# Optimization experiments

Hardware: AMD Instinct MI355X
Metric: run time of the kernel (lower is better)

Reference implementation:

```python
import jax, jax.numpy as jnp
import numpy as np

DIM_H = 128
HEADS = 8
HEAD_DIM = DIM_H // HEADS
N_NODES = 40000
N_EDGES = 640000
BN_EPS = 1e-5


def setup_inputs() -> dict:
    key = jax.random.key(0)
    ks = jax.random.split(key, 16)
    s = 0.05
    x = jax.random.normal(ks[0], (N_NODES, DIM_H), dtype=jnp.float32)
    edge_index = jax.random.randint(ks[1], (2, N_EDGES), 0, N_NODES, dtype=jnp.int64)
    p = lambda k, shp: jax.random.normal(k, shp, dtype=jnp.float32) * s
    return {
        "x": x,
        "edge_index": edge_index,
        "Wk": p(ks[2], (DIM_H, DIM_H)), "bk": p(ks[3], (DIM_H,)),
        "Wv": p(ks[4], (DIM_H, DIM_H)), "bv": p(ks[5], (DIM_H,)),
        "Wo": p(ks[6], (DIM_H, DIM_H)), "bo": p(ks[7], (DIM_H,)),
        "bn1_g": jnp.ones((DIM_H,), jnp.float32), "bn1_b": jnp.zeros((DIM_H,), jnp.float32),
        "W1": p(ks[8], (2 * DIM_H, DIM_H)), "b1": p(ks[9], (2 * DIM_H,)),
        "W2": p(ks[10], (DIM_H, 2 * DIM_H)), "b2": p(ks[11], (DIM_H,)),
        "bn2_g": jnp.ones((DIM_H,), jnp.float32), "bn2_b": jnp.zeros((DIM_H,), jnp.float32),
    }


def _batchnorm(h, gamma, beta):
    # BatchNorm1d in training mode: per-feature batch mean / biased var over nodes
    mu = jnp.mean(h, axis=0)
    var = jnp.mean((h - mu) ** 2, axis=0)
    return (h - mu) * jax.lax.rsqrt(var + BN_EPS) * gamma + beta


def _sparse_attn(x, edge_index, Wk, bk, Wv, bv, Wo, bo):
    N = x.shape[0]
    src, dst = edge_index[0], edge_index[1]
    K = (x @ Wk.T + bk).reshape(N, HEADS, HEAD_DIM)
    V = (x @ Wv.T + bv).reshape(N, HEADS, HEAD_DIM)
    Q = x.reshape(N, HEADS, HEAD_DIM)  # query is raw h (no projection)
    # per-edge scores [E, H]
    scores = jnp.sum(K[src] * Q[dst], axis=-1) / np.sqrt(HEAD_DIM).astype(np.float32)
    # segment softmax over destination nodes (pyg_softmax)
    m = jax.ops.segment_max(scores, dst, num_segments=N)
    e = jnp.exp(scores - m[dst])
    denom = jax.ops.segment_sum(e, dst, num_segments=N)
    attn = e / (denom[dst] + 1e-16)  # [E, H]
    messages = V[src] * attn[:, :, None]  # [E, H, D]
    out = jax.ops.segment_sum(messages, dst, num_segments=N)  # [N, H, D]
    return out.reshape(N, DIM_H) @ Wo.T + bo


def reference(x, edge_index, Wk, bk, Wv, bv, Wo, bo, bn1_g, bn1_b,
              W1, b1, W2, b2, bn2_g, bn2_b):
    h_attn = _sparse_attn(x, edge_index, Wk, bk, Wv, bv, Wo, bo)
    h = _batchnorm(x + h_attn, bn1_g, bn1_b)
    ff = jax.nn.relu(h @ W1.T + b1) @ W2.T + b2
    h = _batchnorm(h + ff, bn2_g, bn2_b)
    return h
```

## Files before the change

kernel.cpp:

```cpp
#include <hip/hip_runtime.h>

#define DIM 128
#define NSHARD 8

typedef __attribute__((ext_vector_type(2))) float f32x2;
typedef __attribute__((ext_vector_type(4))) _Float16 half4;
typedef __attribute__((ext_vector_type(8))) _Float16 half8;
typedef __attribute__((ext_vector_type(4))) float f32x4;

#define HP 136
#define UP 264

__device__ __forceinline__ unsigned char to_fp8(float v) {
  return (unsigned char)(__builtin_amdgcn_cvt_pk_fp8_f32(v, v, 0, false) & 0xff);
}

__global__ __launch_bounds__(256) void conv_wall(const float* __restrict__ Wk,
    const float* __restrict__ Wv, const float* __restrict__ Wo,
    const float* __restrict__ W1, const float* __restrict__ W2,
    _Float16* __restrict__ Wkh, _Float16* __restrict__ Wvh,
    _Float16* __restrict__ Woh, _Float16* __restrict__ W1h,
    _Float16* __restrict__ W2h, int* __restrict__ cnt, float* __restrict__ stats,
    int N) {
  int i = blockIdx.x * 256 + threadIdx.x;
  int nth = gridDim.x * 256;
  if (i < 16384) Wkh[i] = (_Float16)Wk[i];
  else if (i < 32768) Wvh[i - 16384] = (_Float16)Wv[i - 16384];
  else if (i < 49152) Woh[i - 32768] = (_Float16)Wo[i - 32768];
  else if (i < 81920) W1h[i - 49152] = (_Float16)W1[i - 49152];
  else if (i < 114688) W2h[i - 81920] = (_Float16)W2[i - 81920];
  for (int j = i; j < N * NSHARD; j += nth) cnt[j] = 0;
  if (i < 512) stats[i] = 0.f;
}

__global__ __launch_bounds__(256) void kv_mfma(const float* __restrict__ x,
    const _Float16* __restrict__ Wkh, const float* __restrict__ bk,
    const _Float16* __restrict__ Wvh, const float* __restrict__ bv,
    unsigned char* __restrict__ KV8, int N) {
  __shared__ _Float16 xs[64 * HP];
  int tid = threadIdx.x;
  int base = blockIdx.x * 64;
  int lane = tid & 63, w = tid >> 6;
  int l15 = lane & 15, quad = lane >> 4;

  for (int i = tid; i < 64 * 32; i += 256) {
    int m = i >> 5, c4 = i & 31;
    float4 tv = ((const float4*)x)[(size_t)(base + m) * 32 + c4];
    half4 hv;
    hv.x = (_Float16)tv.x; hv.y = (_Float16)tv.y;
    hv.z = (_Float16)tv.z; hv.w = (_Float16)tv.w;
    *(half4*)&xs[m * HP + c4 * 4] = hv;
  }
  __syncthreads();

  half8 afr[4][4];
#pragma unroll
  for (int mt = 0; mt < 4; mt++)
#pragma unroll
    for (int ks = 0; ks < 4; ks++)
      afr[mt][ks] = *(const half8*)&xs[(mt * 16 + l15) * HP + ks * 32 + quad * 8];

  const _Float16* W = (w < 2) ? Wkh : Wvh;
  const float* bias = (w < 2) ? bk : bv;
  int voff = (w < 2) ? 0 : 4;
  int c0 = (w & 1) * 64;

#pragma unroll
  for (int nt = 0; nt < 4; nt++) {
    int f = c0 + nt * 16 + l15;
    half8 bfr[4];
#pragma unroll
    for (int ks = 0; ks < 4; ks++)
      bfr[ks] = *(const half8*)&W[(size_t)f * 128 + ks * 32 + quad * 8];
    f32x4 acc[4];
#pragma unroll
    for (int mt = 0; mt < 4; mt++) acc[mt] = (f32x4){0.f, 0.f, 0.f, 0.f};
#pragma unroll
    for (int ks = 0; ks < 4; ks++)
#pragma unroll
      for (int mt = 0; mt < 4; mt++)
        acc[mt] = __builtin_amdgcn_mfma_f32_16x16x32_f16(afr[mt][ks], bfr[ks],
                                                          acc[mt], 0, 0, 0);
    float bb = bias[f];
    int fo = (f >> 2) * 8 + (f & 3) + voff;
#pragma unroll
    for (int mt = 0; mt < 4; mt++)
#pragma unroll
      for (int r = 0; r < 4; r++)
        KV8[(size_t)(base + mt * 16 + quad * 4 + r) * 256 + fo] =
            to_fp8(acc[mt][r] + bb);
  }
}

__global__ __launch_bounds__(256) void hist_rank(const int* __restrict__ ei,
    int* __restrict__ cnt, int* __restrict__ rank, int N, int E) {
  int e = blockIdx.x * 256 + threadIdx.x;
  if (e < E) rank[e] = atomicAdd(&cnt[(e & (NSHARD - 1)) * N + ei[E + e]], 1);
}

__global__ __launch_bounds__(256) void scanA(const int* __restrict__ cnt,
    int* __restrict__ rs, int* __restrict__ bsum, int N) {
  __shared__ int s[256];
  int t = threadIdx.x;
  int i = blockIdx.x * 256 + t;
  int v = 0;
  if (i < N)
#pragma unroll
    for (int sh = 0; sh < NSHARD; sh++) v += cnt[sh * N + i];
  s[t] = v;
  __syncthreads();
  for (int off = 1; off < 256; off <<= 1) {
    int add = (t >= off) ? s[t - off] : 0;
    __syncthreads();
    s[t] += add;
    __syncthreads();
  }
  if (i < N) rs[i] = s[t] - v;
  if (t == 255) bsum[blockIdx.x] = s[t];
}

__global__ __launch_bounds__(256) void scanB(int* __restrict__ bsum, int nb) {
  __shared__ int s[256];
  int t = threadIdx.x;
  int v = (t < nb) ? bsum[t] : 0;
  s[t] = v;
  __syncthreads();
  for (int off = 1; off < 256; off <<= 1) {
    int add = (t >= off) ? s[t - off] : 0;
    __syncthreads();
    s[t] += add;
    __syncthreads();
  }
  if (t < nb) bsum[t] = s[t] - v;
}

__global__ __launch_bounds__(256) void scanC(int* __restrict__ rs,
    const int* __restrict__ bsum, const int* __restrict__ cnt,
    int* __restrict__ rs_shard, int N, int E) {
  int i = blockIdx.x * 256 + threadIdx.x;
  if (i < N) {
    int b = rs[i] + bsum[blockIdx.x];
    rs[i] = b;
#pragma unroll
    for (int sh = 0; sh < NSHARD; sh++) {
      rs_shard[sh * N + i] = b;
      b += cnt[sh * N + i];
    }
  }
  if (i == 0) rs[N] = E;
}

__global__ __launch_bounds__(256) void scatter2(const int* __restrict__ ei,
    const int* __restrict__ rs_shard, const int* __restrict__ rank,
    int* __restrict__ esrc, int N, int E) {
  int e = blockIdx.x * 256 + threadIdx.x;
  if (e < E)
    esrc[rs_shard[(e & (NSHARD - 1)) * N + ei[E + e]] + rank[e]] = ei[e];
}

__global__ __launch_bounds__(256) void attn_agg(const unsigned char* __restrict__ KV8,
    const float* __restrict__ x, const int* __restrict__ rs,
    const int* __restrict__ esrc, _Float16* __restrict__ attn16, int N) {
  int wave = threadIdx.x >> 6, lane = threadIdx.x & 63;
  int n = blockIdx.x * 4 + wave;
  if (n >= N) return;
  int l = lane & 31, s = lane >> 5;
  float4 q = *(const float4*)&x[(size_t)n * DIM + 4 * l];
  int beg = rs[n], end = rs[n + 1];
  float a0 = 0.f, a1 = 0.f, a2 = 0.f, a3 = 0.f, dloc = 0.f;
  for (int e = beg + s; e < end; e += 8) {
    bool hh[4];
    int ss[4];
#pragma unroll
    for (int u = 0; u < 4; u++) hh[u] = (e + 2 * u) < end;
    ss[0] = esrc[e];
#pragma unroll
    for (int u = 1; u < 4; u++) ss[u] = hh[u] ? esrc[e + 2 * u] : ss[0];
    uint2 kv[4];
#pragma unroll
    for (int u = 0; u < 4; u++)
      kv[u] = *(const uint2*)&KV8[(size_t)ss[u] * 256 + 8 * l];
    float p[4];
#pragma unroll
    for (int u = 0; u < 4; u++) {
      f32x2 k01 = __builtin_amdgcn_cvt_pk_f32_fp8(kv[u].x, false);
      f32x2 k23 = __builtin_amdgcn_cvt_pk_f32_fp8(kv[u].x, true);
      p[u] = k01[0] * q.x + k01[1] * q.y + k23[0] * q.z + k23[1] * q.w;
    }
#pragma unroll
    for (int u = 0; u < 4; u++) p[u] += __shfl_xor(p[u], 1);
#pragma unroll
    for (int u = 0; u < 4; u++) p[u] += __shfl_xor(p[u], 2);
#pragma unroll
    for (int u = 0; u < 4; u++) {
      float ev = hh[u] ? __expf(p[u] * 0.25f) : 0.f;
      dloc += ev;
      f32x2 v01 = __builtin_amdgcn_cvt_pk_f32_fp8(kv[u].y, false);
      f32x2 v23 = __builtin_amdgcn_cvt_pk_f32_fp8(kv[u].y, true);
      a0 += ev * v01[0];
      a1 += ev * v01[1];
      a2 += ev * v23[0];
      a3 += ev * v23[1];
    }
  }
  dloc += __shfl_xor(dloc, 32);
  a0 += __shfl_xor(a0, 32);
  a1 += __shfl_xor(a1, 32);
  a2 += __shfl_xor(a2, 32);
  a3 += __shfl_xor(a3, 32);
  if (s == 0) {
    float inv = 1.0f / (dloc + 1e-16f);
    half4 o;
    o.x = (_Float16)(a0 * inv);
    o.y = (_Float16)(a1 * inv);
    o.z = (_Float16)(a2 * inv);
    o.w = (_Float16)(a3 * inv);
    *(half4*)&attn16[(size_t)n * DIM + 4 * l] = o;
  }
}

__global__ __launch_bounds__(256) void o_proj_mfma(const _Float16* __restrict__ attn16,
    const float* __restrict__ x, const _Float16* __restrict__ Woh,
    const float* __restrict__ bo, float* __restrict__ t,
    float* __restrict__ stats, int N) {
  __shared__ _Float16 as16[64 * HP];
  int tid = threadIdx.x;
  int base = blockIdx.x * 64;
  int lane = tid & 63, w = tid >> 6;
  int l15 = lane & 15, quad = lane >> 4;

  for (int i = tid; i < 64 * 16; i += 256) {
    int m = i >> 4, c8 = i & 15;
    *(half8*)&as16[m * HP + c8 * 8] =
        ((const half8*)attn16)[(size_t)(base + m) * 16 + c8];
  }
  __syncthreads();

  half8 afr[4][4];
#pragma unroll
  for (int mt = 0; mt < 4; mt++)
#pragma unroll
    for (int ks = 0; ks < 4; ks++)
      afr[mt][ks] = *(const half8*)&as16[(mt * 16 + l15) * HP + ks * 32 + quad * 8];

  int c0 = w * 32;
  f32x4 acc[4][2];
#pragma unroll
  for (int mt = 0; mt < 4; mt++)
#pragma unroll
    for (int nt = 0; nt < 2; nt++) acc[mt][nt] = (f32x4){0.f, 0.f, 0.f, 0.f};
#pragma unroll
  for (int ks = 0; ks < 4; ks++) {
    half8 b[2];
#pragma unroll
    for (int nt = 0; nt < 2; nt++)
      b[nt] = *(const half8*)&Woh[(size_t)(c0 + nt * 16 + l15) * 128 + ks * 32 +
                                  quad * 8];
#pragma unroll
    for (int mt = 0; mt < 4; mt++)
#pragma unroll
      for (int nt = 0; nt < 2; nt++)
        acc[mt][nt] =
            __builtin_amdgcn_mfma_f32_16x16x32_f16(afr[mt][ks], b[nt], acc[mt][nt], 0, 0, 0);
  }

#pragma unroll
  for (int nt = 0; nt < 2; nt++) {
    int f = c0 + nt * 16 + l15;
    float bb = bo[f];
    float s = 0.f, q = 0.f;
#pragma unroll
    for (int mt = 0; mt < 4; mt++) {
#pragma unroll
      for (int r = 0; r < 4; r++) {
        int row = mt * 16 + quad * 4 + r;
        float tv = acc[mt][nt][r] + bb + x[(size_t)(base + row) * DIM + f];
        t[(size_t)(base + row) * DIM + f] = tv;
        s += tv;
        q += tv * tv;
      }
    }
    s += __shfl_xor(s, 16);
    s += __shfl_xor(s, 32);
    q += __shfl_xor(q, 16);
    q += __shfl_xor(q, 32);
    if (quad == 0) {
      atomicAdd(&stats[f], s);
      atomicAdd(&stats[128 + f], q);
    }
  }
}

__global__ __launch_bounds__(256) void ffn_mfma(const float* __restrict__ t,
    const float* __restrict__ stats1, const float* __restrict__ g1,
    const float* __restrict__ bb1, const _Float16* __restrict__ W1h,
    const float* __restrict__ b1, const _Float16* __restrict__ W2h,
    const float* __restrict__ b2, float* __restrict__ z,
    float* __restrict__ stats2, float invN, int N) {
  __shared__ _Float16 hs[64 * HP];
  __shared__ _Float16 us[64 * UP];
  __shared__ float cf[256];
  int tid = threadIdx.x;
  int base = blockIdx.x * 64;
  int lane = tid & 63, w = tid >> 6;
  int l15 = lane & 15, quad = lane >> 4;

  if (tid < 128) {
    float mu = stats1[tid] * invN;
    float var = stats1[128 + tid] * invN - mu * mu;
    float a = rsqrtf(var + 1e-5f) * g1[tid];
    cf[tid] = a;
    cf[128 + tid] = bb1[tid] - mu * a;
  }
  __syncthreads();

  for (int i = tid; i < 64 * 32; i += 256) {
    int m = i >> 5, c4 = i & 31;
    float4 tv = ((const float4*)t)[(size_t)(base + m) * 32 + c4];
    float4 ca = ((const float4*)cf)[c4];
    float4 cc = ((const float4*)cf)[32 + c4];
    half4 hv;
    hv.x = (_Float16)(tv.x * ca.x + cc.x);
    hv.y = (_Float16)(tv.y * ca.y + cc.y);
    hv.z = (_Float16)(tv.z * ca.z + cc.z);
    hv.w = (_Float16)(tv.w * ca.w + cc.w);
    *(half4*)&hs[m * HP + c4 * 4] = hv;
  }
  __syncthreads();

  int n0 = w * 64;
  half8 afr[4][4];
#pragma unroll
  for (int mt = 0; mt < 4; mt++)
#pragma unroll
    for (int ks = 0; ks < 4; ks++)
      afr[mt][ks] = *(const half8*)&hs[(mt * 16 + l15) * HP + ks * 32 + quad * 8];

#pragma unroll
  for (int nt = 0; nt < 4; nt++) {
    int n = n0 + nt * 16 + l15;
    half8 bfr[4];
#pragma unroll
    for (int ks = 0; ks < 4; ks++)
      bfr[ks] = *(const half8*)&W1h[(size_t)n * 128 + ks * 32 + quad * 8];
    f32x4 acc[4];
#pragma unroll
    for (int mt = 0; mt < 4; mt++) acc[mt] = (f32x4){0.f, 0.f, 0.f, 0.f};
#pragma unroll
    for (int ks = 0; ks < 4; ks++)
#pragma unroll
      for (int mt = 0; mt < 4; mt++)
        acc[mt] = __builtin_amdgcn_mfma_f32_16x16x32_f16(afr[mt][ks], bfr[ks],
                                                          acc[mt], 0, 0, 0);
    float bias = b1[n];
#pragma unroll
    for (int mt = 0; mt < 4; mt++)
#pragma unroll
      for (int r = 0; r < 4; r++)
        us[(mt * 16 + quad * 4 + r) * UP + n] =
            (_Float16)fmaxf(acc[mt][r] + bias, 0.f);
  }
  __syncthreads();

  int n2 = w * 32;
  f32x4 acc2[4][2];
#pragma unroll
  for (int mt = 0; mt < 4; mt++)
#pragma unroll
    for (int nt = 0; nt < 2; nt++) acc2[mt][nt] = (f32x4){0.f, 0.f, 0.f, 0.f};
  for (int ks = 0; ks < 8; ks++) {
    half8 a[4], b[2];
#pragma unroll
    for (int mt = 0; mt < 4; mt++)
      a[mt] = *(const half8*)&us[(mt * 16 + l15) * UP + ks * 32 + quad * 8];
#pragma unroll
    for (int nt = 0; nt < 2; nt++)
      b[nt] = *(const half8*)&W2h[(size_t)(n2 + nt * 16 + l15) * 256 + ks * 32 +
                                  quad * 8];
#pragma unroll
    for (int mt = 0; mt < 4; mt++)
#pragma unroll
      for (int nt = 0; nt < 2; nt++)
        acc2[mt][nt] =
            __builtin_amdgcn_mfma_f32_16x16x32_f16(a[mt], b[nt], acc2[mt][nt], 0, 0, 0);
  }

#pragma unroll
  for (int nt = 0; nt < 2; nt++) {
    int f = n2 + nt * 16 + l15;
    float bz = b2[f];
    float s = 0.f, q = 0.f;
#pragma unroll
    for (int mt = 0; mt < 4; mt++) {
#pragma unroll
      for (int r = 0; r < 4; r++) {
        int row = mt * 16 + quad * 4 + r;
        float hv = (float)hs[row * HP + f];
        float zv = hv + acc2[mt][nt][r] + bz;
        z[(size_t)(base + row) * DIM + f] = zv;
        s += zv;
        q += zv * zv;
      }
    }
    s += __shfl_xor(s, 16);
    s += __shfl_xor(s, 32);
    q += __shfl_xor(q, 16);
    q += __shfl_xor(q, 32);
    if (quad == 0) {
      atomicAdd(&stats2[f], s);
      atomicAdd(&stats2[128 + f], q);
    }
  }
}

__global__ __launch_bounds__(256) void final_apply(const float* __restrict__ z,
    const float* __restrict__ stats2, const float* __restrict__ g2,
    const float* __restrict__ bb2, float* __restrict__ out, float invN,
    int total4) {
  __shared__ float cf[256];
  int tid = threadIdx.x;
  if (tid < 128) {
    float mu = stats2[tid] * invN;
    float var = stats2[128 + tid] * invN - mu * mu;
    float a = rsqrtf(var + 1e-5f) * g2[tid];
    cf[tid] = a;
    cf[128 + tid] = bb2[tid] - mu * a;
  }
  __syncthreads();
  int i = blockIdx.x * 256 + tid;
  if (i >= total4) return;
  int f = (i * 4) & 127;
  float4 zv = ((const float4*)z)[i];
  float4 o;
  o.x = zv.x * cf[f] + cf[128 + f];
  o.y = zv.y * cf[f + 1] + cf[128 + f + 1];
  o.z = zv.z * cf[f + 2] + cf[128 + f + 2];
  o.w = zv.w * cf[f + 3] + cf[128 + f + 3];
  ((float4*)out)[i] = o;
}

extern "C" void kernel_launch(void* const* d_in, const int* in_sizes, int n_in,
                              void* d_out, int out_size, void* d_ws, size_t ws_size,
                              hipStream_t stream) {
  const float* x = (const float*)d_in[0];
  const int* ei = (const int*)d_in[1];
  const float* Wk = (const float*)d_in[2];
  const float* bk = (const float*)d_in[3];
  const float* Wv = (const float*)d_in[4];
  const float* bv = (const float*)d_in[5];
  const float* Wo = (const float*)d_in[6];
  const float* bo = (const float*)d_in[7];
  const float* bn1_g = (const float*)d_in[8];
  const float* bn1_b = (const float*)d_in[9];
  const float* W1 = (const float*)d_in[10];
  const float* b1 = (const float*)d_in[11];
  const float* W2 = (const float*)d_in[12];
  const float* b2 = (const float*)d_in[13];
  const float* bn2_g = (const float*)d_in[14];
  const float* bn2_b = (const float*)d_in[15];
  float* out = (float*)d_out;

  int N = in_sizes[0] / DIM;
  int E = in_sizes[1] / 2;

  unsigned char* KV8 = (unsigned char*)d_ws;
  _Float16* attn16 = (_Float16*)(KV8 + (size_t)N * 256);
  float* zbuf = (float*)(attn16 + (size_t)N * DIM);
  float* tbuf = zbuf + (size_t)N * DIM;
  _Float16* W1h = (_Float16*)(tbuf + (size_t)N * DIM);
  _Float16* W2h = W1h + 32768;
  _Float16* Wkh = W2h + 32768;
  _Float16* Wvh = Wkh + 16384;
  _Float16* Woh = Wvh + 16384;
  float* stats = (float*)(Woh + 16384);
  int* cnt = (int*)(stats + 512);
  int* rs = cnt + (size_t)N * NSHARD;
  int* rs_shard = rs + N + 1;
  int* rank = rs_shard + (size_t)N * NSHARD;
  int* esrc = rank + E;
  int* bsum = esrc + E;

  int nblk = (N + 255) / 256;
  float invN = 1.0f / N;

  conv_wall<<<512, 256, 0, stream>>>(Wk, Wv, Wo, W1, W2, Wkh, Wvh, Woh, W1h, W2h,
                                     cnt, stats, N);
  kv_mfma<<<N / 64, 256, 0, stream>>>(x, Wkh, bk, Wvh, bv, KV8, N);
  hist_rank<<<(E + 255) / 256, 256, 0, stream>>>(ei, cnt, rank, N, E);
  scanA<<<nblk, 256, 0, stream>>>(cnt, rs, bsum, N);
  scanB<<<1, 256, 0, stream>>>(bsum, nblk);
  scanC<<<nblk, 256, 0, stream>>>(rs, bsum, cnt, rs_shard, N, E);
  scatter2<<<(E + 255) / 256, 256, 0, stream>>>(ei, rs_shard, rank, esrc, N, E);
  attn_agg<<<(N + 3) / 4, 256, 0, stream>>>(KV8, x, rs, esrc, attn16, N);
  o_proj_mfma<<<N / 64, 256, 0, stream>>>(attn16, x, Woh, bo, tbuf, stats, N);
  ffn_mfma<<<N / 64, 256, 0, stream>>>(tbuf, stats, bn1_g, bn1_b, W1h, b1, W2h, b2,
                                       zbuf, stats + 256, invN, N);
  final_apply<<<((N * DIM / 4) + 255) / 256, 256, 0, stream>>>(
      zbuf, stats + 256, bn2_g, bn2_b, out, invN, N * DIM / 4);
}
```

Measured before the change: 249.4 us.

## Store intermediates in fp16, merge scan passes, fuse scatter with KV projection

The pre-BN intermediates t and z are now stored as fp16 instead of fp32, which halves the global traffic between o_proj, ffn and final_apply. The scanB and scanC kernels are merged into one kernel in which every block recomputes the block-sum scan. The edge scatter is fused into the KV projection kernel using extra blocks, removing two launches and letting the two independent jobs overlap. The cost is fp16 rounding of the residual values that feed batchnorm.

```diff
diff --git a/kernel.cpp b/kernel.cpp
--- a/kernel.cpp
+++ b/kernel.cpp
@@ -33,12 +33,78 @@
   if (i < 512) stats[i] = 0.f;
 }
 
-__global__ __launch_bounds__(256) void kv_mfma(const float* __restrict__ x,
+__global__ __launch_bounds__(256) void hist_rank(const int* __restrict__ ei,
+    int* __restrict__ cnt, int* __restrict__ rank, int N, int E) {
+  int e = blockIdx.x * 256 + threadIdx.x;
+  if (e < E) rank[e] = atomicAdd(&cnt[(e & (NSHARD - 1)) * N + ei[E + e]], 1);
+}
+
+__global__ __launch_bounds__(256) void scanA(const int* __restrict__ cnt,
+    int* __restrict__ rs, int* __restrict__ bsum, int N) {
+  __shared__ int s[256];
+  int t = threadIdx.x;
+  int i = blockIdx.x * 256 + t;
+  int v = 0;
+  if (i < N)
+#pragma unroll
+    for (int sh = 0; sh < NSHARD; sh++) v += cnt[sh * N + i];
+  s[t] = v;
+  __syncthreads();
+  for (int off = 1; off < 256; off <<= 1) {
+    int add = (t >= off) ? s[t - off] : 0;
+    __syncthreads();
+    s[t] += add;
+    __syncthreads();
+  }
+  if (i < N) rs[i] = s[t] - v;
+  if (t == 255) bsum[blockIdx.x] = s[t];
+}
+
+__global__ __launch_bounds__(256) void scanBC(int* __restrict__ rs,
+    const int* __restrict__ bsum, const int* __restrict__ cnt,
+    int* __restrict__ rs_shard, int nblk, int N, int E) {
+  __shared__ int s[256];
+  __shared__ int ex[256];
+  int t = threadIdx.x;
+  int v = (t < nblk) ? bsum[t] : 0;
+  s[t] = v;
+  __syncthreads();
+  for (int off = 1; off < 256; off <<= 1) {
+    int add = (t >= off) ? s[t - off] : 0;
+    __syncthreads();
+    s[t] += add;
+    __syncthreads();
+  }
+  ex[t] = s[t] - v;
+  __syncthreads();
+  int boff = ex[blockIdx.x];
+  int i = blockIdx.x * 256 + t;
+  if (i < N) {
+    int b = rs[i] + boff;
+    rs[i] = b;
+#pragma unroll
+    for (int sh = 0; sh < NSHARD; sh++) {
+      rs_shard[sh * N + i] = b;
+      b += cnt[sh * N + i];
+    }
+  }
+  if (i == 0) rs[N] = E;
+}
+
+__global__ __launch_bounds__(256) void scatter_kv(const int* __restrict__ ei,
+    const int* __restrict__ rs_shard, const int* __restrict__ rank,
+    int* __restrict__ esrc, const float* __restrict__ x,
     const _Float16* __restrict__ Wkh, const float* __restrict__ bk,
     const _Float16* __restrict__ Wvh, const float* __restrict__ bv,
-    unsigned char* __restrict__ KV8, int N) {
+    unsigned char* __restrict__ KV8, int kvb, int N, int E) {
   __shared__ _Float16 xs[64 * HP];
   int tid = threadIdx.x;
+  if ((int)blockIdx.x >= kvb) {
+    int e = ((int)blockIdx.x - kvb) * 256 + tid;
+    if (e < E)
+      esrc[rs_shard[(e & (NSHARD - 1)) * N + ei[E + e]] + rank[e]] = ei[e];
+    return;
+  }
   int base = blockIdx.x * 64;
   int lane = tid & 63, w = tid >> 6;
   int l15 = lane & 15, quad = lane >> 4;
@@ -90,72 +156,6 @@
         KV8[(size_t)(base + mt * 16 + quad * 4 + r) * 256 + fo] =
             to_fp8(acc[mt][r] + bb);
   }
-}
-
-__global__ __launch_bounds__(256) void hist_rank(const int* __restrict__ ei,
-    int* __restrict__ cnt, int* __restrict__ rank, int N, int E) {
-  int e = blockIdx.x * 256 + threadIdx.x;
-  if (e < E) rank[e] = atomicAdd(&cnt[(e & (NSHARD - 1)) * N + ei[E + e]], 1);
-}
-
-__global__ __launch_bounds__(256) void scanA(const int* __restrict__ cnt,
-    int* __restrict__ rs, int* __restrict__ bsum, int N) {
-  __shared__ int s[256];
-  int t = threadIdx.x;
-  int i = blockIdx.x * 256 + t;
-  int v = 0;
-  if (i < N)
-#pragma unroll
-    for (int sh = 0; sh < NSHARD; sh++) v += cnt[sh * N + i];
-  s[t] = v;
-  __syncthreads();
-  for (int off = 1; off < 256; off <<= 1) {
-    int add = (t >= off) ? s[t - off] : 0;
-    __syncthreads();
-    s[t] += add;
-    __syncthreads();
-  }
-  if (i < N) rs[i] = s[t] - v;
-  if (t == 255) bsum[blockIdx.x] = s[t];
-}
-
-__global__ __launch_bounds__(256) void scanB(int* __restrict__ bsum, int nb) {
-  __shared__ int s[256];
-  int t = threadIdx.x;
-  int v = (t < nb) ? bsum[t] : 0;
-  s[t] = v;
-  __syncthreads();
-  for (int off = 1; off < 256; off <<= 1) {
-    int add = (t >= off) ? s[t - off] : 0;
-    __syncthreads();
-    s[t] += add;
-    __syncthreads();
-  }
-  if (t < nb) bsum[t] = s[t] - v;
-}
-
-__global__ __launch_bounds__(256) void scanC(int* __restrict__ rs,
-    const int* __restrict__ bsum, const int* __restrict__ cnt,
-    int* __restrict__ rs_shard, int N, int E) {
-  int i = blockIdx.x * 256 + threadIdx.x;
-  if (i < N) {
-    int b = rs[i] + bsum[blockIdx.x];
-    rs[i] = b;
-#pragma unroll
-    for (int sh = 0; sh < NSHARD; sh++) {
-      rs_shard[sh * N + i] = b;
-      b += cnt[sh * N + i];
-    }
-  }
-  if (i == 0) rs[N] = E;
-}
-
-__global__ __launch_bounds__(256) void scatter2(const int* __restrict__ ei,
-    const int* __restrict__ rs_shard, const int* __restrict__ rank,
-    int* __restrict__ esrc, int N, int E) {
-  int e = blockIdx.x * 256 + threadIdx.x;
-  if (e < E)
-    esrc[rs_shard[(e & (NSHARD - 1)) * N + ei[E + e]] + rank[e]] = ei[e];
 }
 
 __global__ __launch_bounds__(256) void attn_agg(const unsigned char* __restrict__ KV8,
@@ -221,7 +221,7 @@
 
 __global__ __launch_bounds__(256) void o_proj_mfma(const _Float16* __restrict__ attn16,
     const float* __restrict__ x, const _Float16* __restrict__ Woh,
-    const float* __restrict__ bo, float* __restrict__ t,
+    const float* __restrict__ bo, _Float16* __restrict__ t16,
     float* __restrict__ stats, int N) {
   __shared__ _Float16 as16[64 * HP];
   int tid = threadIdx.x;
@@ -275,7 +275,7 @@
       for (int r = 0; r < 4; r++) {
         int row = mt * 16 + quad * 4 + r;
         float tv = acc[mt][nt][r] + bb + x[(size_t)(base + row) * DIM + f];
-        t[(size_t)(base + row) * DIM + f] = tv;
+        t16[(size_t)(base + row) * DIM + f] = (_Float16)tv;
         s += tv;
         q += tv * tv;
       }
@@ -291,11 +291,11 @@
   }
 }
 
-__global__ __launch_bounds__(256) void ffn_mfma(const float* __restrict__ t,
+__global__ __launch_bounds__(256) void ffn_mfma(const _Float16* __restrict__ t16,
     const float* __restrict__ stats1, const float* __restrict__ g1,
     const float* __restrict__ bb1, const _Float16* __restrict__ W1h,
     const float* __restrict__ b1, const _Float16* __restrict__ W2h,
-    const float* __restrict__ b2, float* __restrict__ z,
+    const float* __restrict__ b2, _Float16* __restrict__ z16,
     float* __restrict__ stats2, float invN, int N) {
   __shared__ _Float16 hs[64 * HP];
   __shared__ _Float16 us[64 * UP];
@@ -314,17 +314,16 @@
   }
   __syncthreads();
 
-  for (int i = tid; i < 64 * 32; i += 256) {
-    int m = i >> 5, c4 = i & 31;
-    float4 tv = ((const float4*)t)[(size_t)(base + m) * 32 + c4];
-    float4 ca = ((const float4*)cf)[c4];
-    float4 cc = ((const float4*)cf)[32 + c4];
-    half4 hv;
-    hv.x = (_Float16)(tv.x * ca.x + cc.x);
-    hv.y = (_Float16)(tv.y * ca.y + cc.y);
-    hv.z = (_Float16)(tv.z * ca.z + cc.z);
-    hv.w = (_Float16)(tv.w * ca.w + cc.w);
-    *(half4*)&hs[m * HP + c4 * 4] = hv;
+  for (int i = tid; i < 64 * 16; i += 256) {
+    int m = i >> 4, c8 = i & 15;
+    half8 tv = ((const half8*)t16)[(size_t)(base + m) * 16 + c8];
+    half8 hv;
+#pragma unroll
+    for (int j = 0; j < 8; j++) {
+      int f = c8 * 8 + j;
+      hv[j] = (_Float16)((float)tv[j] * cf[f] + cf[128 + f]);
+    }
+    *(half8*)&hs[m * HP + c8 * 8] = hv;
   }
   __syncthreads();
 
@@ -397,7 +396,7 @@
         int row = mt * 16 + quad * 4 + r;
         float hv = (float)hs[row * HP + f];
         float zv = hv + acc2[mt][nt][r] + bz;
-        z[(size_t)(base + row) * DIM + f] = zv;
+        z16[(size_t)(base + row) * DIM + f] = (_Float16)zv;
         s += zv;
         q += zv * zv;
       }
@@ -413,10 +412,10 @@
   }
 }
 
-__global__ __launch_bounds__(256) void final_apply(const float* __restrict__ z,
+__global__ __launch_bounds__(256) void final_apply(const _Float16* __restrict__ z16,
     const float* __restrict__ stats2, const float* __restrict__ g2,
     const float* __restrict__ bb2, float* __restrict__ out, float invN,
-    int total4) {
+    int total8) {
   __shared__ float cf[256];
   int tid = threadIdx.x;
   if (tid < 128) {
@@ -428,15 +427,20 @@
   }
   __syncthreads();
   int i = blockIdx.x * 256 + tid;
-  if (i >= total4) return;
-  int f = (i * 4) & 127;
-  float4 zv = ((const float4*)z)[i];
-  float4 o;
-  o.x = zv.x * cf[f] + cf[128 + f];
-  o.y = zv.y * cf[f + 1] + cf[128 + f + 1];
-  o.z = zv.z * cf[f + 2] + cf[128 + f + 2];
-  o.w = zv.w * cf[f + 3] + cf[128 + f + 3];
-  ((float4*)out)[i] = o;
+  if (i >= total8) return;
+  int f0 = (i * 8) & 127;
+  half8 zv = ((const half8*)z16)[i];
+  float4 o1, o2;
+  o1.x = (float)zv[0] * cf[f0 + 0] + cf[128 + f0 + 0];
+  o1.y = (float)zv[1] * cf[f0 + 1] + cf[128 + f0 + 1];
+  o1.z = (float)zv[2] * cf[f0 + 2] + cf[128 + f0 + 2];
+  o1.w = (float)zv[3] * cf[f0 + 3] + cf[128 + f0 + 3];
+  o2.x = (float)zv[4] * cf[f0 + 4] + cf[128 + f0 + 4];
+  o2.y = (float)zv[5] * cf[f0 + 5] + cf[128 + f0 + 5];
+  o2.z = (float)zv[6] * cf[f0 + 6] + cf[128 + f0 + 6];
+  o2.w = (float)zv[7] * cf[f0 + 7] + cf[128 + f0 + 7];
+  ((float4*)out)[2 * i] = o1;
+  ((float4*)out)[2 * i + 1] = o2;
 }
 
 extern "C" void kernel_launch(void* const* d_in, const int* in_sizes, int n_in,
@@ -465,9 +469,9 @@
 
   unsigned char* KV8 = (unsigned char*)d_ws;
   _Float16* attn16 = (_Float16*)(KV8 + (size_t)N * 256);
-  float* zbuf = (float*)(attn16 + (size_t)N * DIM);
-  float* tbuf = zbuf + (size_t)N * DIM;
-  _Float16* W1h = (_Float16*)(tbuf + (size_t)N * DIM);
+  _Float16* t16 = attn16 + (size_t)N * DIM;
+  _Float16* z16 = t16 + (size_t)N * DIM;
+  _Float16* W1h = z16 + (size_t)N * DIM;
   _Float16* W2h = W1h + 32768;
   _Float16* Wkh = W2h + 32768;
   _Float16* Wvh = Wkh + 16384;
@@ -481,20 +485,22 @@
   int* bsum = esrc + E;
 
   int nblk = (N + 255) / 256;
+  int kvb = N / 64;
+  int sblk = (E + 255) / 256;
   float invN = 1.0f / N;
-
-  conv_wall<<<512, 256, 0, stream>>>(Wk, Wv, Wo, W1, W2, Wkh, Wvh, Woh, W1h, W2h,
-                                     cnt, stats, N);
-  kv_mfma<<<N / 64, 256, 0, stream>>>(x, Wkh, bk, Wvh, bv, KV8, N);
-  hist_rank<<<(E + 255) / 256, 256, 0, stream>>>(ei, cnt, rank, N, E);
+  float* stats2 = stats + 256;
+
+  conv_wall<<<512, 256, 0, stream>>>(Wk, Wv, Wo, W1, W2, Wkh, Wvh, Woh, W1h,
+                                     W2h, cnt, stats, N);
+  hist_rank<<<sblk, 256, 0, stream>>>(ei, cnt, rank, N, E);
   scanA<<<nblk, 256, 0, stream>>>(cnt, rs, bsum, N);
-  scanB<<<1, 256, 0, stream>>>(bsum, nblk);
-  scanC<<<nblk, 256, 0, stream>>>(rs, bsum, cnt, rs_shard, N, E);
-  scatter2<<<(E + 255) / 256, 256, 0, stream>>>(ei, rs_shard, rank, esrc, N, E);
+  scanBC<<<nblk, 256, 0, stream>>>(rs, bsum, cnt, rs_shard, nblk, N, E);
+  scatter_kv<<<kvb + sblk, 256, 0, stream>>>(ei, rs_shard, rank, esrc, x, Wkh,
+                                             bk, Wvh, bv, KV8, kvb, N, E);
   attn_agg<<<(N + 3) / 4, 256, 0, stream>>>(KV8, x, rs, esrc, attn16, N);
-  o_proj_mfma<<<N / 64, 256, 0, stream>>>(attn16, x, Woh, bo, tbuf, stats, N);
-  ffn_mfma<<<N / 64, 256, 0, stream>>>(tbuf, stats, bn1_g, bn1_b, W1h, b1, W2h, b2,
-                                       zbuf, stats + 256, invN, N);
-  final_apply<<<((N * DIM / 4) + 255) / 256, 256, 0, stream>>>(
-      zbuf, stats + 256, bn2_g, bn2_b, out, invN, N * DIM / 4);
-}
+  o_proj_mfma<<<kvb, 256, 0, stream>>>(attn16, x, Woh, bo, t16, stats, N);
+  ffn_mfma<<<kvb, 256, 0, stream>>>(t16, stats, bn1_g, bn1_b, W1h, b1, W2h, b2,
+                                    z16, stats2, invN, N);
+  final_apply<<<((N * DIM / 8) + 255) / 256, 256, 0, stream>>>(
+      z16, stats2, bn2_g, bn2_b, out, invN, N * DIM / 8);
+}
```

Result: faster. 240.2 us (-3.7%).
